# Performance work log

Measured on AMD Instinct MI355X. Metric: run time of the kernel, lower is better.

The kernel has to match this reference:

```python
import jax, jax.numpy as jnp
import numpy as np

D_IN, D_H, D_E, D_MSG, L = 16, 128, 16, 64, 6
N_NODES, N_EDGES, N_GRAPHS = 50000, 1000000, 256
EPS = 1e-5
silu = jax.nn.silu


def _lin(k, fi, fo, shape=None):
    s = shape if shape is not None else (fi, fo)
    return jax.random.normal(k, s, jnp.float32) / np.sqrt(fi)


def setup_inputs() -> dict:
    key = jax.random.key(0)
    ks = iter(jax.random.split(key, 64))
    d = {}
    d['node_feats'] = jax.random.normal(next(ks), (N_NODES, D_IN), jnp.float32)
    d['coords'] = jax.random.normal(next(ks), (N_NODES, 3), jnp.float32)
    d['edge_index'] = jax.random.randint(next(ks), (2, N_EDGES), 0, N_NODES)
    d['edge_feats'] = jax.random.normal(next(ks), (N_EDGES, D_E), jnp.float32)
    d['batch_idx'] = jnp.sort(jax.random.randint(next(ks), (N_NODES,), 0, N_GRAPHS))
    # encoder
    d['enc_w1'] = _lin(next(ks), D_IN, D_H); d['enc_b1'] = jnp.zeros((D_H,), jnp.float32)
    d['enc_w2'] = _lin(next(ks), D_H, D_H); d['enc_b2'] = jnp.zeros((D_H,), jnp.float32)
    # per-layer params, stacked with leading L
    d_msg_in = 2 * D_H + 1 + D_E
    d['pe_w1'] = _lin(next(ks), d_msg_in, D_MSG, (L, d_msg_in, D_MSG)); d['pe_b1'] = jnp.zeros((L, D_MSG), jnp.float32)
    d['pe_w2'] = _lin(next(ks), D_MSG, D_MSG, (L, D_MSG, D_MSG)); d['pe_b2'] = jnp.zeros((L, D_MSG), jnp.float32)
    d['ph_w1'] = _lin(next(ks), D_H + D_MSG, D_H, (L, D_H + D_MSG, D_H)); d['ph_b1'] = jnp.zeros((L, D_H), jnp.float32)
    d['ph_w2'] = _lin(next(ks), D_H, D_H, (L, D_H, D_H)); d['ph_b2'] = jnp.zeros((L, D_H), jnp.float32)
    d['px_w1'] = _lin(next(ks), D_MSG, D_MSG, (L, D_MSG, D_MSG)); d['px_b1'] = jnp.zeros((L, D_MSG), jnp.float32)
    d['px_w2'] = _lin(next(ks), D_MSG, 1, (L, D_MSG, 1)); d['px_b2'] = jnp.zeros((L, 1), jnp.float32)
    d['ln_g'] = jnp.ones((L, D_H), jnp.float32); d['ln_b'] = jnp.zeros((L, D_H), jnp.float32)
    # readout (dropout is inference-mode identity)
    d['ro_w1'] = _lin(next(ks), D_H, D_H); d['ro_b1'] = jnp.zeros((D_H,), jnp.float32)
    d['ro_w2'] = _lin(next(ks), D_H, D_H // 2); d['ro_b2'] = jnp.zeros((D_H // 2,), jnp.float32)
    d['ro_w3'] = _lin(next(ks), D_H // 2, 2); d['ro_b3'] = jnp.zeros((2,), jnp.float32)
    return d


def _layer_norm(x, g, b):
    mu = x.mean(-1, keepdims=True)
    var = ((x - mu) ** 2).mean(-1, keepdims=True)
    return (x - mu) * jax.lax.rsqrt(var + EPS) * g + b


def _egnn_forward(node_feats, coords, edge_index, edge_feats, batch_idx,
                  enc_w1, enc_b1, enc_w2, enc_b2,
                  pe_w1, pe_b1, pe_w2, pe_b2, ph_w1, ph_b1, ph_w2, ph_b2,
                  px_w1, px_b1, px_w2, px_b2, ln_g, ln_b,
                  ro_w1, ro_b1, ro_w2, ro_b2, ro_w3, ro_b3):
    src, dst = edge_index[0], edge_index[1]
    n = node_feats.shape[0]
    h = silu(node_feats @ enc_w1 + enc_b1) @ enc_w2 + enc_b2
    x = coords
    ones_e = jnp.ones((src.shape[0], 1), h.dtype)

    def step(carry, p):
        h, x = carry
        (w1, b1, w2, b2, hw1, hb1, hw2, hb2, xw1, xb1, xw2, xb2, g, b) = p
        diff = x[src] - x[dst]                                   # [E,3]
        sq = (diff ** 2).sum(-1, keepdims=True)                  # [E,1]
        mi = jnp.concatenate([h[src], h[dst], sq, edge_feats], -1)
        msg = silu(silu(mi @ w1 + b1) @ w2 + b2)                 # [E,d_msg]
        count = jnp.maximum(jax.ops.segment_sum(ones_e, dst, num_segments=n), 1.0)
        agg = jax.ops.segment_sum(msg, dst, num_segments=n) / count
        dh = silu(jnp.concatenate([h, agg], -1) @ hw1 + hb1) @ hw2 + hb2
        h_new = _layer_norm(h + dh, g, b)
        w = silu(msg @ xw1 + xb1) @ xw2 + xb2                    # [E,1]
        coord_upd = jax.ops.segment_sum(diff * w, src, num_segments=n) / count
        return (h_new, x + coord_upd), None

    params = (pe_w1, pe_b1, pe_w2, pe_b2, ph_w1, ph_b1, ph_w2, ph_b2,
              px_w1, px_b1, px_w2, px_b2, ln_g, ln_b)
    (h, x), _ = jax.lax.scan(step, (h, x), params)

    gcount = jnp.maximum(jax.ops.segment_sum(jnp.ones((n, 1), h.dtype), batch_idx, num_segments=N_GRAPHS), 1.0)
    graph_h = jax.ops.segment_sum(h, batch_idx, num_segments=N_GRAPHS) / gcount
    r = silu(graph_h @ ro_w1 + ro_b1)
    r = silu(r @ ro_w2 + ro_b2)
    return r @ ro_w3 + ro_b3


def reference(node_feats, coords, edge_index, edge_feats, batch_idx,
              enc_w1, enc_b1, enc_w2, enc_b2,
              pe_w1, pe_b1, pe_w2, pe_b2, ph_w1, ph_b1, ph_w2, ph_b2,
              px_w1, px_b1, px_w2, px_b2, ln_g, ln_b,
              ro_w1, ro_b1, ro_w2, ro_b2, ro_w3, ro_b3):
    return _egnn_forward(node_feats, coords, edge_index, edge_feats, batch_idx,
                         enc_w1, enc_b1, enc_w2, enc_b2,
                         pe_w1, pe_b1, pe_w2, pe_b2, ph_w1, ph_b1, ph_w2, ph_b2,
                         px_w1, px_b1, px_w2, px_b2, ln_g, ln_b,
                         ro_w1, ro_b1, ro_w2, ro_b2, ro_w3, ro_b3)
```

## Files before the change

kernel.cpp:

```cpp
#include <hip/hip_runtime.h>
#include <hip/hip_bf16.h>

#define NN 50000
#define NE 1000000
#define NG 256
#define NL 6
#define NB_SCAN 196
#define EB 128
#define TSTR 66

typedef float v2f __attribute__((ext_vector_type(2)));
typedef short short8 __attribute__((ext_vector_type(8)));
typedef float f32x4 __attribute__((ext_vector_type(4)));

#define MFMA_BF16(a,b,c) __builtin_amdgcn_mfma_f32_16x16x32_bf16(a,b,c,0,0,0)

__device__ __forceinline__ float siluf(float v){
  return v * __builtin_amdgcn_rcpf(1.0f + __expf(-v));
}

__device__ __forceinline__ unsigned f2bf(float x){
  unsigned u = __float_as_uint(x);
  return (u + 0x7FFFu + ((u>>16)&1u)) >> 16;
}
__device__ __forceinline__ float bf2f(unsigned h){
  return __uint_as_float(h<<16);
}

__device__ __forceinline__ unsigned pkhi(unsigned a, unsigned b){
  return __builtin_amdgcn_perm(b, a, 0x07060302u);
}
__device__ __forceinline__ void split4(float v0,float v1,float v2,float v3,
                                       unsigned &h01, unsigned &h23,
                                       unsigned &l01, unsigned &l23){
  unsigned u0=__float_as_uint(v0),u1=__float_as_uint(v1);
  unsigned u2=__float_as_uint(v2),u3=__float_as_uint(v3);
  h01=pkhi(u0,u1); h23=pkhi(u2,u3);
  float r0=v0-__uint_as_float(u0&0xFFFF0000u);
  float r1=v1-__uint_as_float(u1&0xFFFF0000u);
  float r2=v2-__uint_as_float(u2&0xFFFF0000u);
  float r3=v3-__uint_as_float(u3&0xFFFF0000u);
  l01=pkhi(__float_as_uint(r0),__float_as_uint(r1));
  l23=pkhi(__float_as_uint(r2),__float_as_uint(r3));
}

__global__ void k_degrees(const int* __restrict__ ei, int* __restrict__ cnt_dst){
  int e = blockIdx.x*256 + threadIdx.x;
  if (e<NE) atomicAdd(&cnt_dst[ei[NE+e]], 1);
}

__global__ void k_scan1(const int* __restrict__ cnt, int* __restrict__ roff,
                        int* __restrict__ bsum){
  __shared__ int sd[256];
  int t=threadIdx.x; int i=blockIdx.x*256+t;
  int v=(i<NN)?cnt[i]:0;
  sd[t]=v; __syncthreads();
  #pragma unroll
  for(int off=1;off<256;off<<=1){
    int xv=(t>=off)?sd[t-off]:0; __syncthreads();
    sd[t]+=xv; __syncthreads();
  }
  if(i<NN) roff[i]=sd[t]-v;
  if(t==255) bsum[blockIdx.x]=sd[t];
}
__global__ void k_scan2(const int* __restrict__ bsum, int* __restrict__ bbase,
                        int* __restrict__ roff){
  __shared__ int sd[256];
  int t=threadIdx.x;
  int v=(t<NB_SCAN)?bsum[t]:0;
  sd[t]=v; __syncthreads();
  #pragma unroll
  for(int off=1;off<256;off<<=1){
    int xv=(t>=off)?sd[t-off]:0; __syncthreads();
    sd[t]+=xv; __syncthreads();
  }
  if(t<NB_SCAN) bbase[t]=sd[t]-v;
  if(t==255) roff[NN]=sd[t];
}
__global__ void k_scan3(int* __restrict__ roff, const int* __restrict__ bbase){
  int i=blockIdx.x*256+threadIdx.x;
  if(i<NN) roff[i]+=bbase[blockIdx.x];
}

__global__ void k_fill(const int* __restrict__ ei,
                       const int* __restrict__ roff_dst,
                       int* __restrict__ cur_dst, int* __restrict__ dlist){
  int e = blockIdx.x*256 + threadIdx.x;
  if (e<NE){
    int d = ei[NE+e];
    int pd = roff_dst[d] + atomicAdd(&cur_dst[d],1);
    dlist[pd] = e;
  }
}

__global__ void k_gather(const int* __restrict__ ei, const float* __restrict__ ef,
                         const int* __restrict__ dlist,
                         int2* __restrict__ sd_s, unsigned short* __restrict__ efb){
  int p = blockIdx.x*256 + threadIdx.x;
  if (p<NE){
    int e = dlist[p];
    sd_s[p] = make_int2(ei[e], ei[NE+e]);
    int tile = p>>4, l15 = p&15;
    size_t hb = (size_t)tile*512 + (size_t)l15*8;
    const float4* src = (const float4*)(ef + (size_t)e*16);
    #pragma unroll
    for(int q=0;q<4;q++){
      float4 v = src[q];
      float vv[4] = {v.x, v.y, v.z, v.w};
      #pragma unroll
      for(int r=0;r<4;r++){
        int k = q*4+r;
        unsigned h  = f2bf(vv[r]);
        unsigned lo = f2bf(vv[r]-bf2f(h));
        size_t o = hb + (size_t)(k>>3)*128 + (k&7);
        efb[o]     = (unsigned short)h;
        efb[o+256] = (unsigned short)lo;
      }
    }
  }
}

__global__ void k_prep(const float* __restrict__ coords,
                       const int* __restrict__ cnt,
                       float* __restrict__ x, float* __restrict__ cntinv){
  int n = blockIdx.x*256+threadIdx.x;
  if (n<NN){
    x[n*3+0]=coords[n*3+0];
    x[n*3+1]=coords[n*3+1];
    x[n*3+2]=coords[n*3+2];
    cntinv[n]=1.0f/fmaxf((float)cnt[n],1.0f);
  }
}

__global__ void k_wprep(const float* __restrict__ w1full, const float* __restrict__ w2,
                        const float* __restrict__ xw1,
                        unsigned short* __restrict__ blob){
  int t = blockIdx.x*256 + threadIdx.x;
  if (t >= NL*40*64) return;
  int lane = t & 63;
  int f = (t>>6) % 40;
  int l = t / (40*64);
  int m, hl;
  unsigned short* out = blob + (size_t)t*8;
  if (f < 8){
    int mt = f>>1; hl = f&1;
    m = mt*16 + (lane&15);
    int kb = (lane>>4)*8;
    #pragma unroll
    for(int j=0;j<8;j++){
      int k = kb + j;
      float v = (k<16) ? w1full[(size_t)l*273*64 + (size_t)(257+k)*64 + m] : 0.f;
      unsigned h = f2bf(v);
      if (hl) h = f2bf(v - bf2f(h));
      out[j] = (unsigned short)h;
    }
  } else {
    int fi = (f<24) ? (f-8) : (f-24);
    const float* W = ((f<24) ? w2 : xw1) + (size_t)l*4096;
    int mt = fi>>2, kt = (fi>>1)&1; hl = fi&1;
    m = mt*16 + (lane&15);
    int kb = kt*32 + (lane>>4)*8;
    #pragma unroll
    for(int j=0;j<8;j++){
      float v = W[(size_t)(kb+j)*64 + m];
      unsigned h = f2bf(v);
      if (hl) h = f2bf(v - bf2f(h));
      out[j] = (unsigned short)h;
    }
  }
}

__global__ void k_wprep2(const float* __restrict__ pw1, const float* __restrict__ hw1,
                         const float* __restrict__ hw2, unsigned short* __restrict__ blob){
  int t = blockIdx.x*256 + threadIdx.x;
  if (t >= NL*224*64) return;
  int lane = t & 63;
  int f = (t>>6) % 224;
  int l = t / (224*64);
  int m15 = lane & 15, kq = (lane>>4)*8;
  unsigned short* out = blob + (size_t)t*8;
  if (f < 64){
    int mt = f>>3, kt = (f>>1)&3, hl = f&1;
    int m = mt*16 + m15;
    const float* W = pw1 + (size_t)l*273*64;
    #pragma unroll
    for(int j=0;j<8;j++){
      int k = kt*32 + kq + j;
      float v = (m<64) ? W[(size_t)k*64 + m] : W[(size_t)(128+k)*64 + (m-64)];
      unsigned hb = f2bf(v);
      if (hl) hb = f2bf(v - bf2f(hb));
      out[j] = (unsigned short)hb;
    }
  } else if (f < 160){
    int fi = f - 64;
    int mt = fi/12, r = fi%12, kt = r>>1, hl = r&1;
    int m = mt*16 + m15;
    const float* W = hw1 + (size_t)l*192*128;
    #pragma unroll
    for(int j=0;j<8;j++){
      int k = kt*32 + kq + j;
      float v = W[(size_t)k*128 + m];
      unsigned hb = f2bf(v);
      if (hl) hb = f2bf(v - bf2f(hb));
      out[j] = (unsigned short)hb;
    }
  } else {
    int fi = f - 160;
    int mt = fi>>3, kt = (fi>>1)&3, hl = fi&1;
    int m = mt*16 + m15;
    const float* W = hw2 + (size_t)l*128*128;
    #pragma unroll
    for(int j=0;j<8;j++){
      int k = kt*32 + kq + j;
      float v = W[(size_t)k*128 + m];
      unsigned hb = f2bf(v);
      if (hl) hb = f2bf(v - bf2f(hb));
      out[j] = (unsigned short)hb;
    }
  }
}

__global__ void __launch_bounds__(256)
k_encoder(const float* __restrict__ nf,
          const float* __restrict__ w1, const float* __restrict__ b1,
          const float* __restrict__ w2, const float* __restrict__ b2,
          float* __restrict__ h){
  __shared__ float in1[32][17];
  __shared__ float t1[32][129];
  __shared__ float wt[16][136];
  int tid=threadIdx.x;
  int g0=blockIdx.x*32;
  int ty=tid>>4, tx=tid&15;
  int n0=ty*2, n1=ty*2+1;
  { int n=tid>>3, c=(tid&7)*2;
    int gn=g0+n; if(gn>=NN) gn=NN-1;
    float2 v=*(const float2*)(nf+(size_t)gn*16+c);
    in1[n][c]=v.x; in1[n][c+1]=v.y; }
  { int c=tx*8;
    const float* src=w1+(size_t)ty*128+c;
    *(float4*)&wt[ty][c]  =*(const float4*)src;
    *(float4*)&wt[ty][c+4]=*(const float4*)(src+4); }
  __syncthreads();
  float4 a00,a01,a10,a11;
  a00=*(const float4*)(b1+tx*8); a01=*(const float4*)(b1+tx*8+4);
  a10=a00; a11=a01;
  #pragma unroll
  for(int k=0;k<16;k++){
    float m0=in1[n0][k], m1=in1[n1][k];
    float4 wa=*(float4*)&wt[k][tx*8], wb=*(float4*)&wt[k][tx*8+4];
    a00.x+=m0*wa.x; a00.y+=m0*wa.y; a00.z+=m0*wa.z; a00.w+=m0*wa.w;
    a01.x+=m0*wb.x; a01.y+=m0*wb.y; a01.z+=m0*wb.z; a01.w+=m0*wb.w;
    a10.x+=m1*wa.x; a10.y+=m1*wa.y; a10.z+=m1*wa.z; a10.w+=m1*wa.w;
    a11.x+=m1*wb.x; a11.y+=m1*wb.y; a11.z+=m1*wb.z; a11.w+=m1*wb.w;
  }
  int c8=tx*8;
  t1[n0][c8+0]=siluf(a00.x); t1[n0][c8+1]=siluf(a00.y); t1[n0][c8+2]=siluf(a00.z); t1[n0][c8+3]=siluf(a00.w);
  t1[n0][c8+4]=siluf(a01.x); t1[n0][c8+5]=siluf(a01.y); t1[n0][c8+6]=siluf(a01.z); t1[n0][c8+7]=siluf(a01.w);
  t1[n1][c8+0]=siluf(a10.x); t1[n1][c8+1]=siluf(a10.y); t1[n1][c8+2]=siluf(a10.z); t1[n1][c8+3]=siluf(a10.w);
  t1[n1][c8+4]=siluf(a11.x); t1[n1][c8+5]=siluf(a11.y); t1[n1][c8+6]=siluf(a11.z); t1[n1][c8+7]=siluf(a11.w);
  __syncthreads();
  a00=*(const float4*)(b2+c8); a01=*(const float4*)(b2+c8+4);
  a10=a00; a11=a01;
  for(int kt=0;kt<8;kt++){
    { const float* src=w2+(size_t)(kt*16+ty)*128+c8;
      *(float4*)&wt[ty][c8]  =*(const float4*)src;
      *(float4*)&wt[ty][c8+4]=*(const float4*)(src+4); }
    __syncthreads();
    #pragma unroll
    for(int kk=0;kk<16;kk++){
      int k=kt*16+kk;
      float m0=t1[n0][k], m1=t1[n1][k];
      float4 wa=*(float4*)&wt[kk][c8], wb=*(float4*)&wt[kk][c8+4];
      a00.x+=m0*wa.x; a00.y+=m0*wa.y; a00.z+=m0*wa.z; a00.w+=m0*wa.w;
      a01.x+=m0*wb.x; a01.y+=m0*wb.y; a01.z+=m0*wb.z; a01.w+=m0*wb.w;
      a10.x+=m1*wa.x; a10.y+=m1*wa.y; a10.z+=m1*wa.z; a10.w+=m1*wa.w;
      a11.x+=m1*wb.x; a11.y+=m1*wb.y; a11.z+=m1*wb.z; a11.w+=m1*wb.w;
    }
    __syncthreads();
  }
  int gn0=g0+n0, gn1=g0+n1;
  if(gn0<NN){ *(float4*)(h+(size_t)gn0*128+c8)=a00; *(float4*)(h+(size_t)gn0*128+c8+4)=a01; }
  if(gn1<NN){ *(float4*)(h+(size_t)gn1*128+c8)=a10; *(float4*)(h+(size_t)gn1*128+c8+4)=a11; }
}

__device__ __forceinline__ short8 ldB(const unsigned short* base, int row, int kbase){
  const unsigned short* tp = base + row*TSTR + kbase;
  union { unsigned int u[4]; short8 s; } r;
  r.u[0] = *(const unsigned int*)(tp);
  r.u[1] = *(const unsigned int*)(tp+2);
  r.u[2] = *(const unsigned int*)(tp+4);
  r.u[3] = *(const unsigned int*)(tp+6);
  return r.s;
}
__device__ __forceinline__ short8 ldBs(const unsigned short* base, int row, int kbase, int stride){
  const unsigned short* tp = base + row*stride + kbase;
  union { unsigned int u[4]; short8 s; } r;
  r.u[0] = *(const unsigned int*)(tp);
  r.u[1] = *(const unsigned int*)(tp+2);
  r.u[2] = *(const unsigned int*)(tp+4);
  r.u[3] = *(const unsigned int*)(tp+6);
  return r.s;
}

__global__ void __launch_bounds__(256)
k_preM(const float* __restrict__ h, const float* __restrict__ b1,
       const unsigned short* __restrict__ blob,
       float* __restrict__ pa, float* __restrict__ pb){
  __shared__ unsigned short cHi[32*130], cLo[32*130];
  int tid=threadIdx.x;
  int g0=blockIdx.x*32;
  { int n=tid>>3, c0=(tid&7)*16;
    int gn=g0+n; if(gn>=NN) gn=NN-1;
    const float* src=h+(size_t)gn*128+c0;
    #pragma unroll
    for(int q=0;q<4;q++){
      float4 v=*(const float4*)(src+q*4);
      unsigned h01,h23,l01,l23;
      split4(v.x,v.y,v.z,v.w,h01,h23,l01,l23);
      int o=n*130+c0+q*4;
      *(unsigned*)&cHi[o]=h01; *(unsigned*)&cHi[o+2]=h23;
      *(unsigned*)&cLo[o]=l01; *(unsigned*)&cLo[o+2]=l23;
    } }
  __syncthreads();
  int wl=tid>>6, lane=tid&63, q4=lane>>4, l15=lane&15;
  const short8* fr = (const short8*)blob;
  #pragma unroll
  for(int mi=0;mi<2;mi++){
    int mt = wl + mi*4;
    short8 A[4][2];
    #pragma unroll
    for(int kt=0;kt<4;kt++){
      A[kt][0]=fr[(size_t)((mt*4+kt)*2+0)*64+lane];
      A[kt][1]=fr[(size_t)((mt*4+kt)*2+1)*64+lane];
    }
    f32x4 acc0={0.f,0.f,0.f,0.f}, acc1=acc0;
    #pragma unroll
    for(int kt=0;kt<4;kt++){
      short8 bh0=ldBs(cHi, l15,    kt*32+q4*8, 130);
      short8 bl0=ldBs(cLo, l15,    kt*32+q4*8, 130);
      short8 bh1=ldBs(cHi, 16+l15, kt*32+q4*8, 130);
      short8 bl1=ldBs(cLo, 16+l15, kt*32+q4*8, 130);
      acc0=MFMA_BF16(A[kt][0],bh0,acc0); acc0=MFMA_BF16(A[kt][0],bl0,acc0); acc0=MFMA_BF16(A[kt][1],bh0,acc0);
      acc1=MFMA_BF16(A[kt][0],bh1,acc1); acc1=MFMA_BF16(A[kt][0],bl1,acc1); acc1=MFMA_BF16(A[kt][1],bh1,acc1);
    }
    int m0=mt*16+q4*4;
    float4 bias = (mt<4) ? *(const float4*)(b1+m0) : make_float4(0,0,0,0);
    #pragma unroll
    for(int nt=0;nt<2;nt++){
      f32x4 c = nt ? acc1 : acc0;
      int node=g0+nt*16+l15;
      if(node<NN){
        float4 o = make_float4(c[0]+bias.x, c[1]+bias.y, c[2]+bias.z, c[3]+bias.w);
        if (mt<4) *(float4*)(pa+(size_t)node*64+m0)=o;
        else      *(float4*)(pb+(size_t)node*64+(m0-64))=o;
      }
    }
  }
}

__global__ void __launch_bounds__(512,4)
k_edge2(const int2* __restrict__ sd, const unsigned short* __restrict__ efb,
        const float* __restrict__ x,
        const float* __restrict__ pa, const float* __restrict__ pb,
        const int* __restrict__ roff_dst,
        const float* __restrict__ w1,
        const float* __restrict__ b2,
        const float* __restrict__ xb1,
        const float* __restrict__ xw2, const float* __restrict__ xb2,
        const unsigned short* __restrict__ wblob,
        float* __restrict__ agg, float* __restrict__ cacc){
  __shared__ unsigned short tHi[128*TSTR];
  __shared__ unsigned short tLo[128*TSTR];
  __shared__ unsigned short wlds[40*512];
  __shared__ float sqb[128], dxb[128], dyb[128], dzb[128];
  __shared__ int   sbuf[128], dbuf[128];
  int bid = blockIdx.x;
  int nb = (bid&7)*((int)gridDim.x>>3) + (bid>>3);
  int p0 = nb*EB;
  if (p0 >= NE) return;
  int tid = threadIdx.x;
  int wl = tid>>6, lane = tid&63;
  int q4 = lane>>4, l15 = lane&15;

  float4 st0,st1,st2,st3,st4;
  { const float4* wsrc = (const float4*)wblob;
    st0=wsrc[tid]; st1=wsrc[tid+512]; st2=wsrc[tid+1024]; st3=wsrc[tid+1536]; st4=wsrc[tid+2048]; }

  int tile = nb*8 + wl;
  short8 ebh = {0,0,0,0,0,0,0,0};
  short8 ebl = ebh;
  if (lane < 32){
    const short8* ep = (const short8*)efb + (size_t)tile*64;
    ebh = ep[lane]; ebl = ep[lane+32];
  }

  if (tid < 128){
    int p = p0 + tid;
    int2 sdp = (p<NE) ? sd[p] : make_int2(0,0);
    float dx=0.f, dy=0.f, dz=0.f;
    if (p<NE){
      dx = x[sdp.x*3+0]-x[sdp.y*3+0];
      dy = x[sdp.x*3+1]-x[sdp.y*3+1];
      dz = x[sdp.x*3+2]-x[sdp.y*3+2];
    }
    sbuf[tid]=sdp.x; dbuf[tid]=sdp.y;
    sqb[tid]=dx*dx+dy*dy+dz*dz;
    dxb[tid]=dx; dyb[tid]=dy; dzb[tid]=dz;
  }
  { float4* wd = (float4*)wlds;
    wd[tid]=st0; wd[tid+512]=st1; wd[tid+1024]=st2; wd[tid+1536]=st3; wd[tid+2048]=st4; }
  __syncthreads();

  int rowb = 16*wl + l15;
  int s = sbuf[rowb], d = dbuf[rowb];
  float sqv = sqb[rowb];
  const short8* wfr = (const short8*)wlds;

  #pragma unroll
  for(int mt=0;mt<4;mt++){
    short8 ah = wfr[(2*mt+0)*64+lane];
    short8 al = wfr[(2*mt+1)*64+lane];
    f32x4 c = {0.f,0.f,0.f,0.f};
    c = MFMA_BF16(ah, ebh, c);
    c = MFMA_BF16(ah, ebl, c);
    c = MFMA_BF16(al, ebh, c);
    float4 Ai = *(const float4*)(pa + (size_t)s*64 + mt*16 + q4*4);
    float4 Bi = *(const float4*)(pb + (size_t)d*64 + mt*16 + q4*4);
    float4 Wq = *(const float4*)(w1 + 256*64 + mt*16 + q4*4);
    float v0 = siluf(c[0] + Ai.x + Bi.x + sqv*Wq.x);
    float v1 = siluf(c[1] + Ai.y + Bi.y + sqv*Wq.y);
    float v2 = siluf(c[2] + Ai.z + Bi.z + sqv*Wq.z);
    float v3 = siluf(c[3] + Ai.w + Bi.w + sqv*Wq.w);
    unsigned h01,h23,l01,l23;
    split4(v0,v1,v2,v3,h01,h23,l01,l23);
    int mo = rowb*TSTR + mt*16 + q4*4;
    *(unsigned*)&tHi[mo]   = h01;
    *(unsigned*)&tHi[mo+2] = h23;
    *(unsigned*)&tLo[mo]   = l01;
    *(unsigned*)&tLo[mo+2] = l23;
  }

  { short8 bh0 = ldB(tHi, rowb, q4*8);
    short8 bh1 = ldB(tHi, rowb, 32 + q4*8);
    short8 bl0 = ldB(tLo, rowb, q4*8);
    short8 bl1 = ldB(tLo, rowb, 32 + q4*8);
    #pragma unroll
    for(int mt=0;mt<4;mt++){
      short8 ah0 = wfr[(8+mt*4+0)*64+lane];
      short8 al0 = wfr[(8+mt*4+1)*64+lane];
      short8 ah1 = wfr[(8+mt*4+2)*64+lane];
      short8 al1 = wfr[(8+mt*4+3)*64+lane];
      f32x4 c = {0.f,0.f,0.f,0.f};
      c = MFMA_BF16(ah0,bh0,c); c = MFMA_BF16(ah0,bl0,c); c = MFMA_BF16(al0,bh0,c);
      c = MFMA_BF16(ah1,bh1,c); c = MFMA_BF16(ah1,bl1,c); c = MFMA_BF16(al1,bh1,c);
      float4 bb = *(const float4*)(b2 + mt*16 + q4*4);
      float v0=siluf(c[0]+bb.x), v1=siluf(c[1]+bb.y), v2=siluf(c[2]+bb.z), v3=siluf(c[3]+bb.w);
      unsigned h01,h23,l01,l23;
      split4(v0,v1,v2,v3,h01,h23,l01,l23);
      int mo = rowb*TSTR + mt*16 + q4*4;
      *(unsigned*)&tHi[mo]   = h01;
      *(unsigned*)&tHi[mo+2] = h23;
      *(unsigned*)&tLo[mo]   = l01;
      *(unsigned*)&tLo[mo+2] = l23;
    } }

  { short8 mh0 = ldB(tHi, rowb, q4*8);
    short8 mh1 = ldB(tHi, rowb, 32 + q4*8);
    short8 ml0 = ldB(tLo, rowb, q4*8);
    short8 ml1 = ldB(tLo, rowb, 32 + q4*8);
    float part = 0.f;
    #pragma unroll
    for(int mt=0;mt<4;mt++){
      short8 ah0 = wfr[(24+mt*4+0)*64+lane];
      short8 al0 = wfr[(24+mt*4+1)*64+lane];
      short8 ah1 = wfr[(24+mt*4+2)*64+lane];
      short8 al1 = wfr[(24+mt*4+3)*64+lane];
      f32x4 c = {0.f,0.f,0.f,0.f};
      c = MFMA_BF16(ah0,mh0,c); c = MFMA_BF16(ah0,ml0,c); c = MFMA_BF16(al0,mh0,c);
      c = MFMA_BF16(ah1,mh1,c); c = MFMA_BF16(ah1,ml1,c); c = MFMA_BF16(al1,mh1,c);
      float4 xb  = *(const float4*)(xb1 + mt*16 + q4*4);
      float4 wv4 = *(const float4*)(xw2 + mt*16 + q4*4);
      part += siluf(c[0]+xb.x)*wv4.x + siluf(c[1]+xb.y)*wv4.y
            + siluf(c[2]+xb.z)*wv4.z + siluf(c[3]+xb.w)*wv4.w;
    }
    part += __shfl_xor(part,16);
    part += __shfl_xor(part,32);
    int pw = p0 + rowb;
    if (q4==0 && pw < NE){
      float wv = part + xb2[0];
      atomicAdd(&cacc[3*s+0], dxb[rowb]*wv);
      atomicAdd(&cacc[3*s+1], dyb[rowb]*wv);
      atomicAdd(&cacc[3*s+2], dzb[rowb]*wv);
    }
  }
  __syncthreads();

  int pend = (p0+EB < NE) ? (p0+EB) : NE;
  int dfirst = sd[p0].y;
  int dlast  = sd[pend-1].y;
  int jj = (tid&31)*2, slot = tid>>5;
  for (int n=dfirst+slot; n<=dlast; n+=16){
    int rs0 = roff_dst[n], re0 = roff_dst[n+1];
    int rs = (rs0 > p0)   ? rs0 : p0;
    int re = (re0 < pend) ? re0 : pend;
    rs -= p0; re -= p0;
    if (re > rs){
      float s0=0.f, s1=0.f;
      for (int r=rs; r<re; r++){
        unsigned dh = *(const unsigned*)&tHi[r*TSTR+jj];
        unsigned dl = *(const unsigned*)&tLo[r*TSTR+jj];
        s0 += __uint_as_float(dh<<16) + __uint_as_float(dl<<16);
        s1 += __uint_as_float(dh&0xFFFF0000u) + __uint_as_float(dl&0xFFFF0000u);
      }
      if (rs0 >= p0 && re0 <= pend){
        float2 o = make_float2(s0,s1);
        *(float2*)&agg[(size_t)n*64+jj] = o;
      } else {
        atomicAdd(&agg[(size_t)n*64+jj], s0);
        atomicAdd(&agg[(size_t)n*64+jj+1], s1);
      }
    }
  }
}

__global__ void __launch_bounds__(256)
k_nodeM(const float* __restrict__ agg, const float* __restrict__ cacc,
        const float* __restrict__ cntinv,
        const float* __restrict__ hb1, const float* __restrict__ hb2,
        const float* __restrict__ lng, const float* __restrict__ lnb,
        const unsigned short* __restrict__ nbase,
        float* __restrict__ h, float* __restrict__ x){
  __shared__ float hsf[32][132];
  __shared__ unsigned short cHi[32*194], cLo[32*194];
  __shared__ unsigned short t2Hi[32*130], t2Lo[32*130];
  __shared__ float psA[32][8], psB[32][8];
  __shared__ float mu_s[32], rs_s[32];
  int tid=threadIdx.x;
  int g0=blockIdx.x*32;
  { int n=tid>>3, c0=(tid&7)*16;
    int gn=g0+n; if(gn>=NN) gn=NN-1;
    const float* src=h+(size_t)gn*128+c0;
    #pragma unroll
    for(int q=0;q<4;q++){
      float4 v=*(const float4*)(src+q*4);
      *(float4*)&hsf[n][c0+q*4]=v;
      unsigned h01,h23,l01,l23;
      split4(v.x,v.y,v.z,v.w,h01,h23,l01,l23);
      int o=n*194+c0+q*4;
      *(unsigned*)&cHi[o]=h01; *(unsigned*)&cHi[o+2]=h23;
      *(unsigned*)&cLo[o]=l01; *(unsigned*)&cLo[o+2]=l23;
    }
    float ci=cntinv[gn];
    int ca=(tid&7)*8;
    const float* srca=agg+(size_t)gn*64+ca;
    #pragma unroll
    for(int q=0;q<2;q++){
      float4 v=*(const float4*)(srca+q*4);
      unsigned h01,h23,l01,l23;
      split4(v.x*ci,v.y*ci,v.z*ci,v.w*ci,h01,h23,l01,l23);
      int o=n*194+128+ca+q*4;
      *(unsigned*)&cHi[o]=h01; *(unsigned*)&cHi[o+2]=h23;
      *(unsigned*)&cLo[o]=l01; *(unsigned*)&cLo[o+2]=l23;
    } }
  __syncthreads();
  int wl=tid>>6, lane=tid&63, q4=lane>>4, l15=lane&15;
  const short8* f1 = (const short8*)(nbase + 32768);
  const short8* f2 = (const short8*)(nbase + 81920);
  #pragma unroll
  for(int mi=0;mi<2;mi++){
    int mt=wl+mi*4;
    short8 A[6][2];
    #pragma unroll
    for(int kt=0;kt<6;kt++){
      A[kt][0]=f1[(size_t)((mt*6+kt)*2+0)*64+lane];
      A[kt][1]=f1[(size_t)((mt*6+kt)*2+1)*64+lane];
    }
    f32x4 acc0={0.f,0.f,0.f,0.f}, acc1=acc0;
    #pragma unroll
    for(int kt=0;kt<6;kt++){
      short8 bh0=ldBs(cHi, l15,    kt*32+q4*8, 194);
      short8 bl0=ldBs(cLo, l15,    kt*32+q4*8, 194);
      short8 bh1=ldBs(cHi, 16+l15, kt*32+q4*8, 194);
      short8 bl1=ldBs(cLo, 16+l15, kt*32+q4*8, 194);
      acc0=MFMA_BF16(A[kt][0],bh0,acc0); acc0=MFMA_BF16(A[kt][0],bl0,acc0); acc0=MFMA_BF16(A[kt][1],bh0,acc0);
      acc1=MFMA_BF16(A[kt][0],bh1,acc1); acc1=MFMA_BF16(A[kt][0],bl1,acc1); acc1=MFMA_BF16(A[kt][1],bh1,acc1);
    }
    int m0=mt*16+q4*4;
    float4 bias=*(const float4*)(hb1+m0);
    #pragma unroll
    for(int nt=0;nt<2;nt++){
      f32x4 c = nt ? acc1 : acc0;
      int row=nt*16+l15;
      float v0=siluf(c[0]+bias.x), v1=siluf(c[1]+bias.y), v2=siluf(c[2]+bias.z), v3=siluf(c[3]+bias.w);
      unsigned h01,h23,l01,l23;
      split4(v0,v1,v2,v3,h01,h23,l01,l23);
      int mo=row*130+m0;
      *(unsigned*)&t2Hi[mo]=h01; *(unsigned*)&t2Hi[mo+2]=h23;
      *(unsigned*)&t2Lo[mo]=l01; *(unsigned*)&t2Lo[mo+2]=l23;
    }
  }
  __syncthreads();
  #pragma unroll
  for(int mi=0;mi<2;mi++){
    int mt=wl+mi*4;
    short8 A[4][2];
    #pragma unroll
    for(int kt=0;kt<4;kt++){
      A[kt][0]=f2[(size_t)((mt*4+kt)*2+0)*64+lane];
      A[kt][1]=f2[(size_t)((mt*4+kt)*2+1)*64+lane];
    }
    f32x4 acc0={0.f,0.f,0.f,0.f}, acc1=acc0;
    #pragma unroll
    for(int kt=0;kt<4;kt++){
      short8 bh0=ldBs(t2Hi, l15,    kt*32+q4*8, 130);
      short8 bl0=ldBs(t2Lo, l15,    kt*32+q4*8, 130);
      short8 bh1=ldBs(t2Hi, 16+l15, kt*32+q4*8, 130);
      short8 bl1=ldBs(t2Lo, 16+l15, kt*32+q4*8, 130);
      acc0=MFMA_BF16(A[kt][0],bh0,acc0); acc0=MFMA_BF16(A[kt][0],bl0,acc0); acc0=MFMA_BF16(A[kt][1],bh0,acc0);
      acc1=MFMA_BF16(A[kt][0],bh1,acc1); acc1=MFMA_BF16(A[kt][0],bl1,acc1); acc1=MFMA_BF16(A[kt][1],bh1,acc1);
    }
    int m0=mt*16+q4*4;
    float4 bias=*(const float4*)(hb2+m0);
    #pragma unroll
    for(int nt=0;nt<2;nt++){
      f32x4 c = nt ? acc1 : acc0;
      int row=nt*16+l15;
      hsf[row][m0+0]+=c[0]+bias.x;
      hsf[row][m0+1]+=c[1]+bias.y;
      hsf[row][m0+2]+=c[2]+bias.z;
      hsf[row][m0+3]+=c[3]+bias.w;
    }
  }
  __syncthreads();
  { int rid=tid>>3, sub=tid&7;
    float sm=0.f, ss=0.f;
    #pragma unroll
    for(int i=0;i<16;i++){ float v=hsf[rid][sub*16+i]; sm+=v; ss+=v*v; }
    psA[rid][sub]=sm; psB[rid][sub]=ss; }
  __syncthreads();
  { int rid=tid>>3, sub=tid&7;
    if(sub==0){
      float sm=0.f, ss=0.f;
      #pragma unroll
      for(int i=0;i<8;i++){ sm+=psA[rid][i]; ss+=psB[rid][i]; }
      float mu=sm*(1.0f/128.0f);
      float var=ss*(1.0f/128.0f)-mu*mu;
      mu_s[rid]=mu; rs_s[rid]=rsqrtf(fmaxf(var,0.0f)+1e-5f);
    } }
  __syncthreads();
  { int rid=tid>>3, sub=tid&7;
    int gn=g0+rid;
    if(gn<NN){
      float mu=mu_s[rid], rs=rs_s[rid];
      int c0=sub*16;
      #pragma unroll
      for(int q=0;q<4;q++){
        float4 g4=*(const float4*)(lng+c0+q*4);
        float4 b4=*(const float4*)(lnb+c0+q*4);
        float4 o;
        o.x=(hsf[rid][c0+q*4+0]-mu)*rs*g4.x+b4.x;
        o.y=(hsf[rid][c0+q*4+1]-mu)*rs*g4.y+b4.y;
        o.z=(hsf[rid][c0+q*4+2]-mu)*rs*g4.z+b4.z;
        o.w=(hsf[rid][c0+q*4+3]-mu)*rs*g4.w+b4.w;
        *(float4*)(h+(size_t)gn*128+c0+q*4)=o;
      }
    } }
  if(tid<32){
    int gn=g0+tid;
    if(gn<NN){
      float ci=cntinv[gn];
      x[gn*3+0]+=cacc[gn*3+0]*ci;
      x[gn*3+1]+=cacc[gn*3+1]*ci;
      x[gn*3+2]+=cacc[gn*3+2]*ci;
    }
  }
}

__device__ __forceinline__ int lowerb(const int* a, int n, int v){
  int lo=0, hi=n;
  while(lo<hi){ int mid=(lo+hi)>>1; if(a[mid]<v) lo=mid+1; else hi=mid; }
  return lo;
}

__global__ void k_readout(const int* __restrict__ batch, const float* __restrict__ h,
                          const float* __restrict__ w1, const float* __restrict__ b1,
                          const float* __restrict__ w2, const float* __restrict__ b2,
                          const float* __restrict__ w3, const float* __restrict__ b3,
                          float* __restrict__ out){
  int g = blockIdx.x;
  int wl = threadIdx.x>>6, lane = threadIdx.x&63;
  __shared__ float part[4][128];
  __shared__ float gh[128];
  __shared__ float r1[128];
  __shared__ float r2[64];
  int start = lowerb(batch, NN, g);
  int end   = lowerb(batch, NN, g+1);
  float s0=0.f, s1=0.f;
  for(int n=start+wl; n<end; n+=4){
    s0 += h[(size_t)n*128+2*lane];
    s1 += h[(size_t)n*128+2*lane+1];
  }
  part[wl][2*lane]=s0; part[wl][2*lane+1]=s1;
  __syncthreads();
  float ci = 1.0f/fmaxf((float)(end-start),1.0f);
  if(wl==0){
    gh[2*lane]   = (part[0][2*lane]+part[1][2*lane]+part[2][2*lane]+part[3][2*lane])*ci;
    gh[2*lane+1] = (part[0][2*lane+1]+part[1][2*lane+1]+part[2][2*lane+1]+part[3][2*lane+1])*ci;
  }
  __syncthreads();
  if(wl==0){
    float a0=b1[2*lane], a1=b1[2*lane+1];
    for(int k=0;k<128;k++){
      float m=gh[k];
      float2 w=((const float2*)(w1+k*128))[lane];
      a0+=m*w.x; a1+=m*w.y;
    }
    r1[2*lane]=siluf(a0); r1[2*lane+1]=siluf(a1);
  }
  __syncthreads();
  if(wl==0){
    float b=b2[lane];
    for(int k=0;k<128;k++) b += r1[k]*w2[k*64+lane];
    r2[lane]=siluf(b);
  }
  __syncthreads();
  if(wl==0 && lane<2){
    float o=b3[lane];
    for(int k=0;k<64;k++) o += r2[k]*w3[k*2+lane];
    out[g*2+lane]=o;
  }
}

extern "C" void kernel_launch(void* const* d_in, const int* in_sizes, int n_in,
                              void* d_out, int out_size, void* d_ws, size_t ws_size,
                              hipStream_t stream){
  const float* nf     = (const float*)d_in[0];
  const float* coords = (const float*)d_in[1];
  const int*   ei     = (const int*)d_in[2];
  const float* ef     = (const float*)d_in[3];
  const int*   batch  = (const int*)d_in[4];

  const float* enc_w1 = (const float*)d_in[5];
  const float* enc_b1 = (const float*)d_in[6];
  const float* enc_w2 = (const float*)d_in[7];
  const float* enc_b2 = (const float*)d_in[8];
  const float* pe_w1  = (const float*)d_in[9];
  const float* pe_b1  = (const float*)d_in[10];
  const float* pe_w2  = (const float*)d_in[11];
  const float* pe_b2  = (const float*)d_in[12];
  const float* ph_w1  = (const float*)d_in[13];
  const float* ph_b1  = (const float*)d_in[14];
  const float* ph_w2  = (const float*)d_in[15];
  const float* ph_b2  = (const float*)d_in[16];
  const float* px_w1  = (const float*)d_in[17];
  const float* px_b1  = (const float*)d_in[18];
  const float* px_w2  = (const float*)d_in[19];
  const float* px_b2  = (const float*)d_in[20];
  const float* ln_g   = (const float*)d_in[21];
  const float* ln_b   = (const float*)d_in[22];
  const float* ro_w1  = (const float*)d_in[23];
  const float* ro_b1  = (const float*)d_in[24];
  const float* ro_w2  = (const float*)d_in[25];
  const float* ro_b2  = (const float*)d_in[26];
  const float* ro_w3  = (const float*)d_in[27];
  const float* ro_b3  = (const float*)d_in[28];

  char* wsb = (char*)d_ws;
  size_t off = 0;
  auto alloc_f = [&](size_t nfl)->float*{ float* p=(float*)(wsb+off); off+=nfl*4; return p; };
  auto alloc_i = [&](size_t nin)->int*  { int*   p=(int*)(wsb+off);   off+=nin*4; return p; };

  float* h      = alloc_f((size_t)NN*128);
  float* x      = alloc_f((size_t)NN*3);
  float* agg    = alloc_f((size_t)NN*64);
  float* cacc   = alloc_f((size_t)NN*3);
  float* cntinv = alloc_f(NN);
  float* pa     = alloc_f((size_t)NN*64);
  float* pb     = alloc_f((size_t)NN*64);
  unsigned short* efb = (unsigned short*)alloc_f((size_t)NE*16 + 2048);
  int2*  sd_s   = (int2*)alloc_i((size_t)NE*2);
  unsigned short* wblob = (unsigned short*)alloc_i((size_t)NL*40*512/2);
  unsigned short* nblob = (unsigned short*)alloc_i((size_t)NL*224*512/2);
  int* roff_dst = alloc_i(NN+1);
  int* dlist    = alloc_i(NE);
  int* bsum     = alloc_i(256);
  int* bbase    = alloc_i(256);
  int* cnt_dst  = alloc_i(NN);
  int* cur_dst  = alloc_i(NN);

  hipMemsetAsync(cnt_dst, 0, (size_t)2*NN*sizeof(int), stream);
  k_degrees<<<(NE+255)/256,256,0,stream>>>(ei, cnt_dst);
  k_scan1<<<NB_SCAN,256,0,stream>>>(cnt_dst, roff_dst, bsum);
  k_scan2<<<1,256,0,stream>>>(bsum, bbase, roff_dst);
  k_scan3<<<NB_SCAN,256,0,stream>>>(roff_dst, bbase);
  k_fill<<<(NE+255)/256,256,0,stream>>>(ei, roff_dst, cur_dst, dlist);
  k_gather<<<(NE+255)/256,256,0,stream>>>(ei, ef, dlist, sd_s, efb);
  k_prep<<<(NN+255)/256,256,0,stream>>>(coords, cnt_dst, x, cntinv);
  k_wprep<<<(NL*40*64+255)/256,256,0,stream>>>(pe_w1, pe_w2, px_w1, wblob);
  k_wprep2<<<(NL*224*64+255)/256,256,0,stream>>>(pe_w1, ph_w1, ph_w2, nblob);
  k_encoder<<<(NN+31)/32,256,0,stream>>>(nf, enc_w1, enc_b1, enc_w2, enc_b2, h);

  int G  = (NE+EB-1)/EB;
  int G8 = ((G+7)/8)*8;

  for(int l=0;l<NL;l++){
    const unsigned short* nbl = nblob + (size_t)l*224*512;
    k_preM<<<(NN+31)/32,256,0,stream>>>(h, pe_b1+l*64, nbl, pa, pb);
    hipMemsetAsync(agg, 0, (size_t)NN*67*sizeof(float), stream);
    k_edge2<<<G8,512,0,stream>>>(sd_s, efb, x, pa, pb, roff_dst,
        pe_w1+(size_t)l*273*64,
        pe_b2+l*64,
        px_b1+l*64,
        px_w2+l*64, px_b2+l,
        wblob + (size_t)l*40*512,
        agg, cacc);
    k_nodeM<<<(NN+31)/32,256,0,stream>>>(agg, cacc, cntinv,
        ph_b1+l*128, ph_b2+l*128,
        ln_g+l*128, ln_b+l*128, nbl, h, x);
  }

  k_readout<<<NG,256,0,stream>>>(batch, h,
      ro_w1, ro_b1, ro_w2, ro_b2, ro_w3, ro_b3, (float*)d_out);
}
```

Before: 1.902 ms.

## Replace per-edge coordinate atomics with a source-CSR segmented reduction

The edge kernel no longer does three scattered float atomics per edge into the per-source coordinate accumulator. It writes each edge's coordinate update into a dense per-edge buffer. A new kernel then sums these per source node through a source-sorted CSR built once in preprocessing (extra degree count, scan and fill). This removes random-address atomic contention, at the cost of a 16 MB per-edge buffer, an extra gather pass and one more launch per layer. Summation order also becomes deterministic.

```diff
diff --git a/kernel.cpp b/kernel.cpp
--- a/kernel.cpp
+++ b/kernel.cpp
@@ -44,9 +44,13 @@
   l23=pkhi(__float_as_uint(r2),__float_as_uint(r3));
 }
 
-__global__ void k_degrees(const int* __restrict__ ei, int* __restrict__ cnt_dst){
+__global__ void k_degrees(const int* __restrict__ ei, int* __restrict__ cnt_dst,
+                          int* __restrict__ cnt_src){
   int e = blockIdx.x*256 + threadIdx.x;
-  if (e<NE) atomicAdd(&cnt_dst[ei[NE+e]], 1);
+  if (e<NE){
+    atomicAdd(&cnt_dst[ei[NE+e]], 1);
+    atomicAdd(&cnt_src[ei[e]], 1);
+  }
 }
 
 __global__ void k_scan1(const int* __restrict__ cnt, int* __restrict__ roff,
@@ -83,13 +87,17 @@
 }
 
 __global__ void k_fill(const int* __restrict__ ei,
-                       const int* __restrict__ roff_dst,
-                       int* __restrict__ cur_dst, int* __restrict__ dlist){
+                       const int* __restrict__ roff_dst, const int* __restrict__ roff_src,
+                       int* __restrict__ cur_dst, int* __restrict__ cur_src,
+                       int* __restrict__ dlist, int* __restrict__ slist){
   int e = blockIdx.x*256 + threadIdx.x;
   if (e<NE){
     int d = ei[NE+e];
     int pd = roff_dst[d] + atomicAdd(&cur_dst[d],1);
     dlist[pd] = e;
+    int s = ei[e];
+    int ps = roff_src[s] + atomicAdd(&cur_src[s],1);
+    slist[ps] = pd;
   }
 }
 
@@ -368,7 +376,7 @@
         const float* __restrict__ xb1,
         const float* __restrict__ xw2, const float* __restrict__ xb2,
         const unsigned short* __restrict__ wblob,
-        float* __restrict__ agg, float* __restrict__ cacc){
+        float* __restrict__ agg, float4* __restrict__ cvec){
   __shared__ unsigned short tHi[128*TSTR];
   __shared__ unsigned short tLo[128*TSTR];
   __shared__ unsigned short wlds[40*512];
@@ -488,9 +496,7 @@
     int pw = p0 + rowb;
     if (q4==0 && pw < NE){
       float wv = part + xb2[0];
-      atomicAdd(&cacc[3*s+0], dxb[rowb]*wv);
-      atomicAdd(&cacc[3*s+1], dyb[rowb]*wv);
-      atomicAdd(&cacc[3*s+2], dzb[rowb]*wv);
+      cvec[pw] = make_float4(dxb[rowb]*wv, dyb[rowb]*wv, dzb[rowb]*wv, 0.f);
     }
   }
   __syncthreads();
@@ -523,6 +529,29 @@
   }
 }
 
+__global__ void k_coordC(const int* __restrict__ roff_src, const int* __restrict__ slist,
+                         const float4* __restrict__ cvec, float* __restrict__ cacc){
+  int tid=threadIdx.x;
+  int grp=tid>>4, sub=tid&15;
+  int n = blockIdx.x*16 + grp;
+  if (n >= NN) return;
+  int s = roff_src[n], e2 = roff_src[n+1];
+  float a0=0.f, a1=0.f, a2=0.f;
+  for (int p=s+sub; p<e2; p+=16){
+    float4 c = cvec[slist[p]];
+    a0 += c.x; a1 += c.y; a2 += c.z;
+  }
+  #pragma unroll
+  for(int off=1; off<16; off<<=1){
+    a0 += __shfl_xor(a0, off);
+    a1 += __shfl_xor(a1, off);
+    a2 += __shfl_xor(a2, off);
+  }
+  if (sub==0){
+    cacc[n*3+0]=a0; cacc[n*3+1]=a1; cacc[n*3+2]=a2;
+  }
+}
+
 __global__ void __launch_bounds__(256)
 k_nodeM(const float* __restrict__ agg, const float* __restrict__ cacc,
         const float* __restrict__ cntinv,
@@ -777,23 +806,31 @@
   float* cntinv = alloc_f(NN);
   float* pa     = alloc_f((size_t)NN*64);
   float* pb     = alloc_f((size_t)NN*64);
+  float4* cvec  = (float4*)alloc_f((size_t)NE*4);
   unsigned short* efb = (unsigned short*)alloc_f((size_t)NE*16 + 2048);
   int2*  sd_s   = (int2*)alloc_i((size_t)NE*2);
   unsigned short* wblob = (unsigned short*)alloc_i((size_t)NL*40*512/2);
   unsigned short* nblob = (unsigned short*)alloc_i((size_t)NL*224*512/2);
   int* roff_dst = alloc_i(NN+1);
+  int* roff_src = alloc_i(NN+1);
   int* dlist    = alloc_i(NE);
+  int* slist    = alloc_i(NE);
   int* bsum     = alloc_i(256);
   int* bbase    = alloc_i(256);
   int* cnt_dst  = alloc_i(NN);
+  int* cnt_src  = alloc_i(NN);
   int* cur_dst  = alloc_i(NN);
-
-  hipMemsetAsync(cnt_dst, 0, (size_t)2*NN*sizeof(int), stream);
-  k_degrees<<<(NE+255)/256,256,0,stream>>>(ei, cnt_dst);
+  int* cur_src  = alloc_i(NN);
+
+  hipMemsetAsync(cnt_dst, 0, (size_t)4*NN*sizeof(int), stream);
+  k_degrees<<<(NE+255)/256,256,0,stream>>>(ei, cnt_dst, cnt_src);
   k_scan1<<<NB_SCAN,256,0,stream>>>(cnt_dst, roff_dst, bsum);
   k_scan2<<<1,256,0,stream>>>(bsum, bbase, roff_dst);
   k_scan3<<<NB_SCAN,256,0,stream>>>(roff_dst, bbase);
-  k_fill<<<(NE+255)/256,256,0,stream>>>(ei, roff_dst, cur_dst, dlist);
+  k_scan1<<<NB_SCAN,256,0,stream>>>(cnt_src, roff_src, bsum);
+  k_scan2<<<1,256,0,stream>>>(bsum, bbase, roff_src);
+  k_scan3<<<NB_SCAN,256,0,stream>>>(roff_src, bbase);
+  k_fill<<<(NE+255)/256,256,0,stream>>>(ei, roff_dst, roff_src, cur_dst, cur_src, dlist, slist);
   k_gather<<<(NE+255)/256,256,0,stream>>>(ei, ef, dlist, sd_s, efb);
   k_prep<<<(NN+255)/256,256,0,stream>>>(coords, cnt_dst, x, cntinv);
   k_wprep<<<(NL*40*64+255)/256,256,0,stream>>>(pe_w1, pe_w2, px_w1, wblob);
@@ -806,14 +843,15 @@
   for(int l=0;l<NL;l++){
     const unsigned short* nbl = nblob + (size_t)l*224*512;
     k_preM<<<(NN+31)/32,256,0,stream>>>(h, pe_b1+l*64, nbl, pa, pb);
-    hipMemsetAsync(agg, 0, (size_t)NN*67*sizeof(float), stream);
+    hipMemsetAsync(agg, 0, (size_t)NN*64*sizeof(float), stream);
     k_edge2<<<G8,512,0,stream>>>(sd_s, efb, x, pa, pb, roff_dst,
         pe_w1+(size_t)l*273*64,
         pe_b2+l*64,
         px_b1+l*64,
         px_w2+l*64, px_b2+l,
         wblob + (size_t)l*40*512,
-        agg, cacc);
+        agg, cvec);
+    k_coordC<<<(NN+15)/16,256,0,stream>>>(roff_src, slist, cvec, cacc);
     k_nodeM<<<(NN+31)/32,256,0,stream>>>(agg, cacc, cntinv,
         ph_b1+l*128, ph_b2+l*128,
         ln_g+l*128, ln_b+l*128, nbl, h, x);
```

Measured after the change: 1.821 ms. 1.04x faster.
